# Optimization experiments

Hardware: AMD Instinct MI355X
Metric: run time of the kernel (lower is better)

## Reference

```python
import jax, jax.numpy as jnp
import numpy as np

N_FEATS = 512
SND = N_FEATS // 2
N_NODES = 100000
NUM_GRAPHS = 256
EPS = 1e-5


def graph_norm(x, batch, num_seg, w, b, ms):
    # PyG GraphNorm: out = w * (x - mean[batch]*mean_scale) / sqrt(var[batch]+eps) + b
    cnt = jax.ops.segment_sum(jnp.ones((x.shape[0],), x.dtype), batch, num_seg)
    cnt = jnp.maximum(cnt, 1.0)[:, None]
    mean = jax.ops.segment_sum(x, batch, num_seg) / cnt
    sub = x - mean[batch] * ms
    var = jax.ops.segment_sum(sub * sub, batch, num_seg) / cnt
    return w * sub * jax.lax.rsqrt(var[batch] + EPS) + b


def graph_norm_global(x, w, b, ms):
    # gn3 is called without `batch` in the source -> batch=None -> global stats
    mean = jnp.mean(x, axis=0, keepdims=True)
    sub = x - mean * ms
    var = jnp.mean(sub * sub, axis=0, keepdims=True)
    return w * sub * jax.lax.rsqrt(var + EPS) + b


def prelu(x, a):
    return jnp.where(x >= 0, x, a * x)


def linear(x, W, b):
    return x @ W.T + b


def setup_inputs() -> dict:
    key = jax.random.key(0)
    ks = jax.random.split(key, 12)
    d = {}
    d['x'] = jax.random.normal(ks[0], (N_NODES, N_FEATS), jnp.float32)
    d['batch'] = jnp.sort(jax.random.randint(ks[1], (N_NODES,), 0, NUM_GRAPHS)).astype(jnp.int64)
    # GraphNorm params (PyG init: weight=1, bias=0, mean_scale=1)
    for name, dim in [('gn1', N_FEATS), ('gn2', SND), ('gn3', SND), ('gn4', SND), ('gn5', SND)]:
        d[name + '_w'] = jnp.ones((dim,), jnp.float32)
        d[name + '_b'] = jnp.zeros((dim,), jnp.float32)
        d[name + '_ms'] = jnp.ones((dim,), jnp.float32)
    # Linear weights/biases
    d['lin1_W'] = jax.random.normal(ks[2], (SND, N_FEATS), jnp.float32) * 0.02
    d['lin1_b'] = jnp.zeros((SND,), jnp.float32)
    d['lin2_W'] = jax.random.normal(ks[3], (SND, SND), jnp.float32) * 0.02
    d['lin2_b'] = jnp.zeros((SND,), jnp.float32)
    d['lin3_W'] = jax.random.normal(ks[4], (SND, SND), jnp.float32) * 0.02
    d['lin3_b'] = jnp.zeros((SND,), jnp.float32)
    d['lin4_W'] = jax.random.normal(ks[5], (SND, SND), jnp.float32) * 0.02
    d['lin4_b'] = jnp.zeros((SND,), jnp.float32)
    d['lin5_W'] = jax.random.normal(ks[6], (N_FEATS, SND), jnp.float32) * 0.02
    d['lin5_b'] = jnp.zeros((N_FEATS,), jnp.float32)
    # PReLU params (single param, init 0.25)
    for name in ['a2', 'a3', 'a4', 'a5']:
        d[name] = jnp.full((1,), 0.25, jnp.float32)
    return d


def reference(x, batch,
              gn1_w, gn1_b, gn1_ms, gn2_w, gn2_b, gn2_ms, gn3_w, gn3_b, gn3_ms,
              gn4_w, gn4_b, gn4_ms, gn5_w, gn5_b, gn5_ms,
              lin1_W, lin1_b, lin2_W, lin2_b, lin3_W, lin3_b, lin4_W, lin4_b,
              lin5_W, lin5_b, a2, a3, a4, a5):
    # x = lin1(gn1(x, batch))
    x1 = linear(graph_norm(x, batch, NUM_GRAPHS, gn1_w, gn1_b, gn1_ms), lin1_W, lin1_b)
    # x = (lin3(gn3(lin2(gn2(x, batch)))) + x) / 2   [gn3 uses global stats]
    h = linear(prelu(graph_norm(x1, batch, NUM_GRAPHS, gn2_w, gn2_b, gn2_ms), a2), lin2_W, lin2_b)
    h = linear(prelu(graph_norm_global(h, gn3_w, gn3_b, gn3_ms), a3), lin3_W, lin3_b)
    x2 = (h + x1) / 2
    # x = (lin4(gn4(x, batch)) + x) / 2
    h = linear(prelu(graph_norm(x2, batch, NUM_GRAPHS, gn4_w, gn4_b, gn4_ms), a4), lin4_W, lin4_b)
    x3 = (h + x2) / 2
    # x = lin5(gn5(x, batch))
    out = linear(prelu(graph_norm(x3, batch, NUM_GRAPHS, gn5_w, gn5_b, gn5_ms), a5), lin5_W, lin5_b)
    return out
```

## Files before the change

### kernel.cpp

```cpp
#include <hip/hip_runtime.h>
#include <cstddef>
#include <cstdint>

#define NF 512
#define SND 256
#define NG 256
#define EPSV 1e-5f

typedef __attribute__((ext_vector_type(8))) short bf16x8;
typedef __attribute__((ext_vector_type(4))) float f32x4;

__device__ __forceinline__ float bf2f(unsigned short u) {
  return __uint_as_float(((unsigned int)u) << 16);
}
__device__ __forceinline__ unsigned short f2bf(float f) {
  unsigned int u = __float_as_uint(f);
  return (unsigned short)((u + 0x7fffu + ((u >> 16) & 1u)) >> 16);
}
__device__ __forceinline__ unsigned int pack2bf(float a, float b) {
  return (unsigned int)f2bf(a) | ((unsigned int)f2bf(b) << 16);
}

__device__ __forceinline__ void async16(const unsigned short* g, unsigned short* l) {
  __builtin_amdgcn_global_load_lds(
      (const __attribute__((address_space(1))) unsigned int*)g,
      (__attribute__((address_space(3))) unsigned int*)l, 16, 0, 0);
}

__global__ void offsets_kernel(const int* __restrict__ batch, int* __restrict__ offs, int M) {
  int t = threadIdx.x + blockIdx.x * blockDim.x;
  if (t > NG) return;
  if (t == NG) { offs[NG] = M; return; }
  int lo = 0, hi = M;
  while (lo < hi) { int mid = (lo + hi) >> 1; if (batch[mid] < t) lo = mid + 1; else hi = mid; }
  offs[t] = lo;
}

__global__ void wconv_kernel(const float* __restrict__ w1, const float* __restrict__ w2,
                             const float* __restrict__ w3, const float* __restrict__ w4,
                             const float* __restrict__ w5,
                             unsigned short* __restrict__ o1, unsigned short* __restrict__ o2,
                             unsigned short* __restrict__ o3, unsigned short* __restrict__ o4,
                             unsigned short* __restrict__ o5) {
  int i = threadIdx.x + blockIdx.x * 256;
  if (i < 131072) { o1[i] = f2bf(w1[i]); o5[i] = f2bf(w5[i]); }
  if (i < 65536)  { o2[i] = f2bf(w2[i]); o3[i] = f2bf(w3[i]); o4[i] = f2bf(w4[i]); }
}

template <typename T, int F, int VE, bool WB, bool GLOB>
__global__ void stats_k(const T* __restrict__ X, const int* __restrict__ offs, int M,
                        float* __restrict__ ps, float* __restrict__ pq,
                        unsigned short* __restrict__ xbf) {
  constexpr int TPR = F / VE, RPB = 256 / TPR;
  const int g = GLOB ? 0 : blockIdx.x;
  const int s = GLOB ? 0 : offs[g];
  const int e = GLOB ? M : offs[g + 1];
  const int slot = threadIdx.x / TPR;
  const int f0 = (threadIdx.x % TPR) * VE;
  float a0[VE], a1[VE];
#pragma unroll
  for (int i = 0; i < VE; ++i) { a0[i] = 0.f; a1[i] = 0.f; }

  for (int r = s + (int)blockIdx.y * RPB + slot; r < e; r += (int)gridDim.y * RPB) {
    float v[VE];
    if constexpr (sizeof(T) == 2) {
      const uint4 u = *(const uint4*)((const unsigned short*)X + (size_t)r * F + f0);
      v[0] = __uint_as_float(u.x << 16); v[1] = __uint_as_float(u.x & 0xffff0000u);
      v[2] = __uint_as_float(u.y << 16); v[3] = __uint_as_float(u.y & 0xffff0000u);
      v[4] = __uint_as_float(u.z << 16); v[5] = __uint_as_float(u.z & 0xffff0000u);
      v[6] = __uint_as_float(u.w << 16); v[7] = __uint_as_float(u.w & 0xffff0000u);
    } else {
      const float4 u = *(const float4*)((const float*)X + (size_t)r * F + f0);
      v[0] = u.x; v[1] = u.y; v[2] = u.z; v[3] = u.w;
    }
#pragma unroll
    for (int i = 0; i < VE; ++i) { a0[i] += v[i]; a1[i] += v[i] * v[i]; }
    if constexpr (WB) {
      *(uint2*)(xbf + (size_t)r * F + f0) = make_uint2(pack2bf(v[0], v[1]), pack2bf(v[2], v[3]));
    }
  }

  const int groups = GLOB ? 1 : (int)gridDim.x;
  const size_t pbase = (size_t)blockIdx.y * ((size_t)groups * F) + (size_t)g * F + f0;

  __shared__ float red[256 * VE];
  __syncthreads();
#pragma unroll
  for (int i = 0; i < VE; ++i) red[slot * F + f0 + i] = a0[i];
  __syncthreads();
  if (slot == 0) {
    float t[VE];
#pragma unroll
    for (int i = 0; i < VE; ++i) {
      t[i] = 0.f;
      for (int sl = 0; sl < RPB; ++sl) t[i] += red[sl * F + f0 + i];
    }
#pragma unroll
    for (int i = 0; i < VE; i += 4)
      *(float4*)&ps[pbase + i] = make_float4(t[i], t[i + 1], t[i + 2], t[i + 3]);
  }
  __syncthreads();
#pragma unroll
  for (int i = 0; i < VE; ++i) red[slot * F + f0 + i] = a1[i];
  __syncthreads();
  if (slot == 0) {
    float t[VE];
#pragma unroll
    for (int i = 0; i < VE; ++i) {
      t[i] = 0.f;
      for (int sl = 0; sl < RPB; ++sl) t[i] += red[sl * F + f0 + i];
    }
#pragma unroll
    for (int i = 0; i < VE; i += 4)
      *(float4*)&pq[pbase + i] = make_float4(t[i], t[i + 1], t[i + 2], t[i + 3]);
  }
}

__global__ void finalize_kernel(const float* __restrict__ ps, const float* __restrict__ pq,
                                const float* __restrict__ w, const float* __restrict__ b,
                                const float* __restrict__ ms, const int* __restrict__ offs,
                                int fixed_cnt, int F, int P,
                                float* __restrict__ sc, float* __restrict__ sh) {
  int idx = threadIdx.x + blockIdx.x * 256;
  int g = idx / F, f = idx - g * F;
  int total = (int)gridDim.x * 256;
  float s0 = 0.f, s1 = 0.f;
  for (int p = 0; p < P; ++p) {
    s0 += ps[(size_t)p * total + idx];
    s1 += pq[(size_t)p * total + idx];
  }
  float cnt = offs ? (float)(offs[g + 1] - offs[g]) : (float)fixed_cnt;
  cnt = fmaxf(cnt, 1.0f);
  float mean = s0 / cnt;
  float ex2  = s1 / cnt;
  float mm = mean * ms[f];
  float var = ex2 - 2.f * mm * mean + mm * mm;
  float rstd = rsqrtf(var + EPSV);
  float s = w[f] * rstd;
  sc[idx] = s;
  sh[idx] = b[f] - mm * s;
}

template <int K, bool PRELU, bool GLOB>
__global__ void norm_act(const unsigned short* __restrict__ Xin, unsigned short* __restrict__ Aout,
                         const float* __restrict__ SC, const float* __restrict__ SH,
                         const int* __restrict__ batch, const float* __restrict__ pa, int M) {
  constexpr int TPR = K / 8, RPB = 256 / TPR;
  const int row = blockIdx.x * RPB + threadIdx.x / TPR;
  if (row >= M) return;
  const int f0 = (threadIdx.x % TPR) * 8;
  const int g = GLOB ? 0 : batch[row];
  const float a = PRELU ? pa[0] : 0.f;
  const uint4 u = *(const uint4*)(Xin + (size_t)row * K + f0);
  const float4 s0 = *(const float4*)(SC + (size_t)g * K + f0);
  const float4 s1 = *(const float4*)(SC + (size_t)g * K + f0 + 4);
  const float4 h0 = *(const float4*)(SH + (size_t)g * K + f0);
  const float4 h1 = *(const float4*)(SH + (size_t)g * K + f0 + 4);
  float v[8];
  v[0] = __uint_as_float(u.x << 16); v[1] = __uint_as_float(u.x & 0xffff0000u);
  v[2] = __uint_as_float(u.y << 16); v[3] = __uint_as_float(u.y & 0xffff0000u);
  v[4] = __uint_as_float(u.z << 16); v[5] = __uint_as_float(u.z & 0xffff0000u);
  v[6] = __uint_as_float(u.w << 16); v[7] = __uint_as_float(u.w & 0xffff0000u);
  v[0] = fmaf(v[0], s0.x, h0.x); v[1] = fmaf(v[1], s0.y, h0.y);
  v[2] = fmaf(v[2], s0.z, h0.z); v[3] = fmaf(v[3], s0.w, h0.w);
  v[4] = fmaf(v[4], s1.x, h1.x); v[5] = fmaf(v[5], s1.y, h1.y);
  v[6] = fmaf(v[6], s1.z, h1.z); v[7] = fmaf(v[7], s1.w, h1.w);
  if (PRELU) {
#pragma unroll
    for (int i = 0; i < 8; ++i) v[i] = v[i] >= 0.f ? v[i] : a * v[i];
  }
  *(uint4*)(Aout + (size_t)row * K + f0) =
      make_uint4(pack2bf(v[0], v[1]), pack2bf(v[2], v[3]),
                 pack2bf(v[4], v[5]), pack2bf(v[6], v[7]));
}

template <int K, bool RESID, bool OUT_BF>
__global__ __launch_bounds__(256, 4)
void gemm_bf16(const unsigned short* __restrict__ A, const unsigned short* __restrict__ Bw,
               const float* __restrict__ lb_, const unsigned short* __restrict__ resid,
               void* __restrict__ outv, int M, int N) {
  __shared__ __align__(16) unsigned short sA[128 * 64];
  __shared__ __align__(16) unsigned short sB[128 * 64];
  const int tid = threadIdx.x;
  const int wave = tid >> 6, lane = tid & 63;
  const int m0 = blockIdx.y * 128, n0 = blockIdx.x * 128;
  const int wm = wave & 1, wn = wave >> 1;
  const int qd = lane >> 4, l15 = lane & 15;

  const int srow = lane >> 3;
  const int schunk = lane & 7;
  const int gchunk = schunk ^ srow;

  f32x4 acc[4][4];
#pragma unroll
  for (int mi = 0; mi < 4; ++mi)
#pragma unroll
    for (int ni = 0; ni < 4; ++ni) acc[mi][ni] = (f32x4){0.f, 0.f, 0.f, 0.f};

  const unsigned short* Abase = A + (size_t)m0 * K;
  const unsigned short* Bbase = Bw + (size_t)n0 * K;

  for (int kt = 0; kt < K / 64; ++kt) {
    const int kOff = kt * 64 + gchunk * 8;
#pragma unroll
    for (int i = 0; i < 4; ++i) {
      const int r = wave * 32 + i * 8 + srow;
      async16(Abase + (size_t)r * K + kOff, &sA[(wave * 4 + i) * 512]);
      async16(Bbase + (size_t)r * K + kOff, &sB[(wave * 4 + i) * 512]);
    }
    __syncthreads();
#pragma unroll
    for (int ks = 0; ks < 2; ++ks) {
      bf16x8 af[4], bfr[4];
      const int pc = ((ks * 4 + qd) ^ (l15 & 7)) * 8;
#pragma unroll
      for (int mi = 0; mi < 4; ++mi)
        af[mi] = *(const bf16x8*)&sA[(wm * 64 + mi * 16 + l15) * 64 + pc];
#pragma unroll
      for (int ni = 0; ni < 4; ++ni)
        bfr[ni] = *(const bf16x8*)&sB[(wn * 64 + ni * 16 + l15) * 64 + pc];
#pragma unroll
      for (int mi = 0; mi < 4; ++mi)
#pragma unroll
        for (int ni = 0; ni < 4; ++ni)
          acc[mi][ni] = __builtin_amdgcn_mfma_f32_16x16x32_bf16(af[mi], bfr[ni], acc[mi][ni], 0, 0, 0);
    }
    __syncthreads();
  }

  float lb[4];
#pragma unroll
  for (int ni = 0; ni < 4; ++ni) lb[ni] = lb_[n0 + wn * 64 + ni * 16 + l15];
  float* outF = (float*)outv;
  unsigned short* outH = (unsigned short*)outv;
#pragma unroll
  for (int mi = 0; mi < 4; ++mi) {
#pragma unroll
    for (int i = 0; i < 4; ++i) {
      const int row = m0 + wm * 64 + mi * 16 + qd * 4 + i;
      if (row >= M) continue;
#pragma unroll
      for (int ni = 0; ni < 4; ++ni) {
        const int col = n0 + wn * 64 + ni * 16 + l15;
        float v = acc[mi][ni][i] + lb[ni];
        if (RESID) v = 0.5f * (v + bf2f(resid[(size_t)row * N + col]));
        if (OUT_BF) outH[(size_t)row * N + col] = f2bf(v);
        else        outF[(size_t)row * N + col] = v;
      }
    }
  }
}

extern "C" void kernel_launch(void* const* d_in, const int* in_sizes, int n_in,
                              void* d_out, int out_size, void* d_ws, size_t ws_size,
                              hipStream_t stream) {
  const float* x    = (const float*)d_in[0];
  const int* batch  = (const int*)d_in[1];
  const float* gw1 = (const float*)d_in[2],  *gb1 = (const float*)d_in[3],  *gm1 = (const float*)d_in[4];
  const float* gw2 = (const float*)d_in[5],  *gb2 = (const float*)d_in[6],  *gm2 = (const float*)d_in[7];
  const float* gw3 = (const float*)d_in[8],  *gb3 = (const float*)d_in[9],  *gm3 = (const float*)d_in[10];
  const float* gw4 = (const float*)d_in[11], *gb4 = (const float*)d_in[12], *gm4 = (const float*)d_in[13];
  const float* gw5 = (const float*)d_in[14], *gb5 = (const float*)d_in[15], *gm5 = (const float*)d_in[16];
  const float* W1 = (const float*)d_in[17], *b1 = (const float*)d_in[18];
  const float* W2 = (const float*)d_in[19], *b2 = (const float*)d_in[20];
  const float* W3 = (const float*)d_in[21], *b3 = (const float*)d_in[22];
  const float* W4 = (const float*)d_in[23], *b4 = (const float*)d_in[24];
  const float* W5 = (const float*)d_in[25], *b5 = (const float*)d_in[26];
  const float* a2 = (const float*)d_in[27], *a3 = (const float*)d_in[28];
  const float* a4 = (const float*)d_in[29], *a5 = (const float*)d_in[30];
  float* out = (float*)d_out;
  (void)n_in; (void)out_size; (void)ws_size;

  const int M = in_sizes[0] / NF;
  const int MT = (M + 127) / 128;
  const int M_pad = MT * 128;

  char* wsp = (char*)d_ws;
  size_t off = 0;
  auto take = [&](size_t bytes) -> void* {
    void* p = wsp + off;
    off = (off + bytes + 255) & ~(size_t)255;
    return p;
  };
  int* offs            = (int*)take((NG + 1) * sizeof(int));
  unsigned short* Wb1  = (unsigned short*)take((size_t)SND * NF * 2);
  unsigned short* Wb2  = (unsigned short*)take((size_t)SND * SND * 2);
  unsigned short* Wb3  = (unsigned short*)take((size_t)SND * SND * 2);
  unsigned short* Wb4  = (unsigned short*)take((size_t)SND * SND * 2);
  unsigned short* Wb5  = (unsigned short*)take((size_t)NF * SND * 2);
  float* psum          = (float*)take((size_t)8 * NG * NF * 4);
  float* psq           = (float*)take((size_t)8 * NG * NF * 4);
  float* sc            = (float*)take((size_t)NG * NF * 4);
  float* sh            = (float*)take((size_t)NG * NF * 4);
  unsigned short* B1   = (unsigned short*)take((size_t)M_pad * SND * 2);
  unsigned short* B2   = (unsigned short*)take((size_t)M_pad * SND * 2);
  unsigned short* Abuf = (unsigned short*)take((size_t)M_pad * NF * 2);

  offsets_kernel<<<2, 256, 0, stream>>>(batch, offs, M);
  wconv_kernel<<<512, 256, 0, stream>>>(W1, W2, W3, W4, W5, Wb1, Wb2, Wb3, Wb4, Wb5);

  stats_k<float, NF, 4, true, false><<<dim3(NG, 8), 256, 0, stream>>>(x, offs, M, psum, psq, Abuf);
  finalize_kernel<<<(NG * NF) / 256, 256, 0, stream>>>(psum, psq, gw1, gb1, gm1, offs, M, NF, 8, sc, sh);
  norm_act<NF, false, false><<<(M + 3) / 4, 256, 0, stream>>>(Abuf, Abuf, sc, sh, batch, nullptr, M);
  gemm_bf16<NF, false, true><<<dim3(SND / 128, MT), 256, 0, stream>>>(Abuf, Wb1, b1, nullptr, B1, M, SND);

  stats_k<unsigned short, SND, 8, false, false><<<dim3(NG, 4), 256, 0, stream>>>(B1, offs, M, psum, psq, nullptr);
  finalize_kernel<<<(NG * SND) / 256, 256, 0, stream>>>(psum, psq, gw2, gb2, gm2, offs, M, SND, 4, sc, sh);
  norm_act<SND, true, false><<<(M + 7) / 8, 256, 0, stream>>>(B1, Abuf, sc, sh, batch, a2, M);
  gemm_bf16<SND, false, true><<<dim3(SND / 128, MT), 256, 0, stream>>>(Abuf, Wb2, b2, nullptr, B2, M, SND);

  stats_k<unsigned short, SND, 8, false, true><<<dim3(1, 512), 256, 0, stream>>>(B2, offs, M, psum, psq, nullptr);
  finalize_kernel<<<1, 256, 0, stream>>>(psum, psq, gw3, gb3, gm3, nullptr, M, SND, 512, sc, sh);
  norm_act<SND, true, true><<<(M + 7) / 8, 256, 0, stream>>>(B2, Abuf, sc, sh, nullptr, a3, M);
  gemm_bf16<SND, true, true><<<dim3(SND / 128, MT), 256, 0, stream>>>(Abuf, Wb3, b3, B1, B2, M, SND);

  stats_k<unsigned short, SND, 8, false, false><<<dim3(NG, 4), 256, 0, stream>>>(B2, offs, M, psum, psq, nullptr);
  finalize_kernel<<<(NG * SND) / 256, 256, 0, stream>>>(psum, psq, gw4, gb4, gm4, offs, M, SND, 4, sc, sh);
  norm_act<SND, true, false><<<(M + 7) / 8, 256, 0, stream>>>(B2, Abuf, sc, sh, batch, a4, M);
  gemm_bf16<SND, true, true><<<dim3(SND / 128, MT), 256, 0, stream>>>(Abuf, Wb4, b4, B2, B1, M, SND);

  stats_k<unsigned short, SND, 8, false, false><<<dim3(NG, 4), 256, 0, stream>>>(B1, offs, M, psum, psq, nullptr);
  finalize_kernel<<<(NG * SND) / 256, 256, 0, stream>>>(psum, psq, gw5, gb5, gm5, offs, M, SND, 4, sc, sh);
  norm_act<SND, true, false><<<(M + 7) / 8, 256, 0, stream>>>(B1, Abuf, sc, sh, batch, a5, M);
  gemm_bf16<SND, false, false><<<dim3(NF / 128, MT), 256, 0, stream>>>(Abuf, Wb5, b5, nullptr, out, M, NF);
}
```

Before: 912.1 us.

## Fuse finalize into stats via last-block atomics, merge prep kernels, remap GEMM tiles per XCD

After: 1.474 ms. 1.62x slower.

```diff
diff --git a/kernel.cpp b/kernel.cpp
--- a/kernel.cpp
+++ b/kernel.cpp
@@ -20,6 +20,12 @@
 __device__ __forceinline__ unsigned int pack2bf(float a, float b) {
   return (unsigned int)f2bf(a) | ((unsigned int)f2bf(b) << 16);
 }
+__device__ __forceinline__ void unpack8(const uint4 u, float* v) {
+  v[0] = __uint_as_float(u.x << 16); v[1] = __uint_as_float(u.x & 0xffff0000u);
+  v[2] = __uint_as_float(u.y << 16); v[3] = __uint_as_float(u.y & 0xffff0000u);
+  v[4] = __uint_as_float(u.z << 16); v[5] = __uint_as_float(u.z & 0xffff0000u);
+  v[6] = __uint_as_float(u.w << 16); v[7] = __uint_as_float(u.w & 0xffff0000u);
+}
 
 __device__ __forceinline__ void async16(const unsigned short* g, unsigned short* l) {
   __builtin_amdgcn_global_load_lds(
@@ -27,30 +33,36 @@
       (__attribute__((address_space(3))) unsigned int*)l, 16, 0, 0);
 }
 
-__global__ void offsets_kernel(const int* __restrict__ batch, int* __restrict__ offs, int M) {
-  int t = threadIdx.x + blockIdx.x * blockDim.x;
-  if (t > NG) return;
-  if (t == NG) { offs[NG] = M; return; }
-  int lo = 0, hi = M;
-  while (lo < hi) { int mid = (lo + hi) >> 1; if (batch[mid] < t) lo = mid + 1; else hi = mid; }
-  offs[t] = lo;
-}
-
-__global__ void wconv_kernel(const float* __restrict__ w1, const float* __restrict__ w2,
-                             const float* __restrict__ w3, const float* __restrict__ w4,
-                             const float* __restrict__ w5,
-                             unsigned short* __restrict__ o1, unsigned short* __restrict__ o2,
-                             unsigned short* __restrict__ o3, unsigned short* __restrict__ o4,
-                             unsigned short* __restrict__ o5) {
+__global__ void prep_kernel(const float* __restrict__ w1, const float* __restrict__ w2,
+                            const float* __restrict__ w3, const float* __restrict__ w4,
+                            const float* __restrict__ w5,
+                            unsigned short* __restrict__ o1, unsigned short* __restrict__ o2,
+                            unsigned short* __restrict__ o3, unsigned short* __restrict__ o4,
+                            unsigned short* __restrict__ o5,
+                            const int* __restrict__ batch, int* __restrict__ offs, int M,
+                            unsigned int* __restrict__ cnts) {
   int i = threadIdx.x + blockIdx.x * 256;
   if (i < 131072) { o1[i] = f2bf(w1[i]); o5[i] = f2bf(w5[i]); }
   if (i < 65536)  { o2[i] = f2bf(w2[i]); o3[i] = f2bf(w3[i]); o4[i] = f2bf(w4[i]); }
+  if (i < 5 * NG) cnts[i] = 0u;
+  if (i <= NG) {
+    if (i == NG) { offs[NG] = M; }
+    else {
+      int lo = 0, hi = M;
+      while (lo < hi) { int mid = (lo + hi) >> 1; if (batch[mid] < i) lo = mid + 1; else hi = mid; }
+      offs[i] = lo;
+    }
+  }
 }
 
 template <typename T, int F, int VE, bool WB, bool GLOB>
 __global__ void stats_k(const T* __restrict__ X, const int* __restrict__ offs, int M,
                         float* __restrict__ ps, float* __restrict__ pq,
-                        unsigned short* __restrict__ xbf) {
+                        unsigned short* __restrict__ xbf,
+                        const float* __restrict__ w, const float* __restrict__ bb,
+                        const float* __restrict__ ms,
+                        float* __restrict__ sc, float* __restrict__ sh,
+                        unsigned int* __restrict__ cnt) {
   constexpr int TPR = F / VE, RPB = 256 / TPR;
   const int g = GLOB ? 0 : blockIdx.x;
   const int s = GLOB ? 0 : offs[g];
@@ -65,10 +77,7 @@
     float v[VE];
     if constexpr (sizeof(T) == 2) {
       const uint4 u = *(const uint4*)((const unsigned short*)X + (size_t)r * F + f0);
-      v[0] = __uint_as_float(u.x << 16); v[1] = __uint_as_float(u.x & 0xffff0000u);
-      v[2] = __uint_as_float(u.y << 16); v[3] = __uint_as_float(u.y & 0xffff0000u);
-      v[4] = __uint_as_float(u.z << 16); v[5] = __uint_as_float(u.z & 0xffff0000u);
-      v[6] = __uint_as_float(u.w << 16); v[7] = __uint_as_float(u.w & 0xffff0000u);
+      unpack8(u, v);
     } else {
       const float4 u = *(const float4*)((const float*)X + (size_t)r * F + f0);
       v[0] = u.x; v[1] = u.y; v[2] = u.z; v[3] = u.w;
@@ -114,31 +123,35 @@
     for (int i = 0; i < VE; i += 4)
       *(float4*)&pq[pbase + i] = make_float4(t[i], t[i + 1], t[i + 2], t[i + 3]);
   }
-}
-
-__global__ void finalize_kernel(const float* __restrict__ ps, const float* __restrict__ pq,
-                                const float* __restrict__ w, const float* __restrict__ b,
-                                const float* __restrict__ ms, const int* __restrict__ offs,
-                                int fixed_cnt, int F, int P,
-                                float* __restrict__ sc, float* __restrict__ sh) {
-  int idx = threadIdx.x + blockIdx.x * 256;
-  int g = idx / F, f = idx - g * F;
-  int total = (int)gridDim.x * 256;
-  float s0 = 0.f, s1 = 0.f;
-  for (int p = 0; p < P; ++p) {
-    s0 += ps[(size_t)p * total + idx];
-    s1 += pq[(size_t)p * total + idx];
-  }
-  float cnt = offs ? (float)(offs[g + 1] - offs[g]) : (float)fixed_cnt;
-  cnt = fmaxf(cnt, 1.0f);
-  float mean = s0 / cnt;
-  float ex2  = s1 / cnt;
-  float mm = mean * ms[f];
-  float var = ex2 - 2.f * mm * mean + mm * mm;
-  float rstd = rsqrtf(var + EPSV);
-  float s = w[f] * rstd;
-  sc[idx] = s;
-  sh[idx] = b[f] - mm * s;
+
+  __shared__ bool lastBlk;
+  __threadfence();
+  __syncthreads();
+  if (threadIdx.x == 0)
+    lastBlk = (atomicAdd(&cnt[g], 1u) == (unsigned)gridDim.y - 1u);
+  __syncthreads();
+  if (!lastBlk) return;
+  __threadfence();
+
+  const int P = (int)gridDim.y;
+  const float cntf = fmaxf((float)(e - s), 1.0f);
+  const size_t stride = (size_t)groups * F;
+  for (int f = threadIdx.x; f < F; f += 256) {
+    float s0 = 0.f, s1 = 0.f;
+    const size_t base = (size_t)g * F + f;
+    for (int p = 0; p < P; ++p) {
+      s0 += ps[(size_t)p * stride + base];
+      s1 += pq[(size_t)p * stride + base];
+    }
+    float mean = s0 / cntf;
+    float ex2  = s1 / cntf;
+    float mm = mean * ms[f];
+    float var = ex2 - 2.f * mm * mean + mm * mm;
+    float rstd = rsqrtf(var + EPSV);
+    float sv = w[f] * rstd;
+    sc[g * F + f] = sv;
+    sh[g * F + f] = bb[f] - mm * sv;
+  }
 }
 
 template <int K, bool PRELU, bool GLOB>
@@ -157,10 +170,7 @@
   const float4 h0 = *(const float4*)(SH + (size_t)g * K + f0);
   const float4 h1 = *(const float4*)(SH + (size_t)g * K + f0 + 4);
   float v[8];
-  v[0] = __uint_as_float(u.x << 16); v[1] = __uint_as_float(u.x & 0xffff0000u);
-  v[2] = __uint_as_float(u.y << 16); v[3] = __uint_as_float(u.y & 0xffff0000u);
-  v[4] = __uint_as_float(u.z << 16); v[5] = __uint_as_float(u.z & 0xffff0000u);
-  v[6] = __uint_as_float(u.w << 16); v[7] = __uint_as_float(u.w & 0xffff0000u);
+  unpack8(u, v);
   v[0] = fmaf(v[0], s0.x, h0.x); v[1] = fmaf(v[1], s0.y, h0.y);
   v[2] = fmaf(v[2], s0.z, h0.z); v[3] = fmaf(v[3], s0.w, h0.w);
   v[4] = fmaf(v[4], s1.x, h1.x); v[5] = fmaf(v[5], s1.y, h1.y);
@@ -183,7 +193,17 @@
   __shared__ __align__(16) unsigned short sB[128 * 64];
   const int tid = threadIdx.x;
   const int wave = tid >> 6, lane = tid & 63;
-  const int m0 = blockIdx.y * 128, n0 = blockIdx.x * 128;
+
+  const int gx = (int)gridDim.x;
+  const int nwg = gx * (int)gridDim.y;
+  const int bid = (int)blockIdx.y * gx + (int)blockIdx.x;
+  const int q = nwg >> 3, r = nwg & 7;
+  const int xcd = bid & 7, ii = bid >> 3;
+  const int logical = (xcd < r) ? xcd * (q + 1) + ii : r * (q + 1) + (xcd - r) * q + ii;
+  const int bx = logical % gx;
+  const int by = logical / gx;
+
+  const int m0 = by * 128, n0 = bx * 128;
   const int wm = wave & 1, wn = wave >> 1;
   const int qd = lane >> 4, l15 = lane & 15;
 
@@ -204,9 +224,9 @@
     const int kOff = kt * 64 + gchunk * 8;
 #pragma unroll
     for (int i = 0; i < 4; ++i) {
-      const int r = wave * 32 + i * 8 + srow;
-      async16(Abase + (size_t)r * K + kOff, &sA[(wave * 4 + i) * 512]);
-      async16(Bbase + (size_t)r * K + kOff, &sB[(wave * 4 + i) * 512]);
+      const int r2 = wave * 32 + i * 8 + srow;
+      async16(Abase + (size_t)r2 * K + kOff, &sA[(wave * 4 + i) * 512]);
+      async16(Bbase + (size_t)r2 * K + kOff, &sB[(wave * 4 + i) * 512]);
     }
     __syncthreads();
 #pragma unroll
@@ -283,6 +303,7 @@
     return p;
   };
   int* offs            = (int*)take((NG + 1) * sizeof(int));
+  unsigned int* cnts   = (unsigned int*)take((size_t)5 * NG * sizeof(unsigned int));
   unsigned short* Wb1  = (unsigned short*)take((size_t)SND * NF * 2);
   unsigned short* Wb2  = (unsigned short*)take((size_t)SND * SND * 2);
   unsigned short* Wb3  = (unsigned short*)take((size_t)SND * SND * 2);
@@ -296,31 +317,31 @@
   unsigned short* B2   = (unsigned short*)take((size_t)M_pad * SND * 2);
   unsigned short* Abuf = (unsigned short*)take((size_t)M_pad * NF * 2);
 
-  offsets_kernel<<<2, 256, 0, stream>>>(batch, offs, M);
-  wconv_kernel<<<512, 256, 0, stream>>>(W1, W2, W3, W4, W5, Wb1, Wb2, Wb3, Wb4, Wb5);
-
-  stats_k<float, NF, 4, true, false><<<dim3(NG, 8), 256, 0, stream>>>(x, offs, M, psum, psq, Abuf);
-  finalize_kernel<<<(NG * NF) / 256, 256, 0, stream>>>(psum, psq, gw1, gb1, gm1, offs, M, NF, 8, sc, sh);
+  prep_kernel<<<512, 256, 0, stream>>>(W1, W2, W3, W4, W5, Wb1, Wb2, Wb3, Wb4, Wb5,
+                                       batch, offs, M, cnts);
+
+  stats_k<float, NF, 4, true, false><<<dim3(NG, 8), 256, 0, stream>>>(
+      x, offs, M, psum, psq, Abuf, gw1, gb1, gm1, sc, sh, cnts + 0 * NG);
   norm_act<NF, false, false><<<(M + 3) / 4, 256, 0, stream>>>(Abuf, Abuf, sc, sh, batch, nullptr, M);
   gemm_bf16<NF, false, true><<<dim3(SND / 128, MT), 256, 0, stream>>>(Abuf, Wb1, b1, nullptr, B1, M, SND);
 
-  stats_k<unsigned short, SND, 8, false, false><<<dim3(NG, 4), 256, 0, stream>>>(B1, offs, M, psum, psq, nullptr);
-  finalize_kernel<<<(NG * SND) / 256, 256, 0, stream>>>(psum, psq, gw2, gb2, gm2, offs, M, SND, 4, sc, sh);
+  stats_k<unsigned short, SND, 8, false, false><<<dim3(NG, 4), 256, 0, stream>>>(
+      B1, offs, M, psum, psq, nullptr, gw2, gb2, gm2, sc, sh, cnts + 1 * NG);
   norm_act<SND, true, false><<<(M + 7) / 8, 256, 0, stream>>>(B1, Abuf, sc, sh, batch, a2, M);
   gemm_bf16<SND, false, true><<<dim3(SND / 128, MT), 256, 0, stream>>>(Abuf, Wb2, b2, nullptr, B2, M, SND);
 
-  stats_k<unsigned short, SND, 8, false, true><<<dim3(1, 512), 256, 0, stream>>>(B2, offs, M, psum, psq, nullptr);
-  finalize_kernel<<<1, 256, 0, stream>>>(psum, psq, gw3, gb3, gm3, nullptr, M, SND, 512, sc, sh);
+  stats_k<unsigned short, SND, 8, false, true><<<dim3(1, 512), 256, 0, stream>>>(
+      B2, offs, M, psum, psq, nullptr, gw3, gb3, gm3, sc, sh, cnts + 2 * NG);
   norm_act<SND, true, true><<<(M + 7) / 8, 256, 0, stream>>>(B2, Abuf, sc, sh, nullptr, a3, M);
   gemm_bf16<SND, true, true><<<dim3(SND / 128, MT), 256, 0, stream>>>(Abuf, Wb3, b3, B1, B2, M, SND);
 
-  stats_k<unsigned short, SND, 8, false, false><<<dim3(NG, 4), 256, 0, stream>>>(B2, offs, M, psum, psq, nullptr);
-  finalize_kernel<<<(NG * SND) / 256, 256, 0, stream>>>(psum, psq, gw4, gb4, gm4, offs, M, SND, 4, sc, sh);
+  stats_k<unsigned short, SND, 8, false, false><<<dim3(NG, 4), 256, 0, stream>>>(
+      B2, offs, M, psum, psq, nullptr, gw4, gb4, gm4, sc, sh, cnts + 3 * NG);
   norm_act<SND, true, false><<<(M + 7) / 8, 256, 0, stream>>>(B2, Abuf, sc, sh, batch, a4, M);
   gemm_bf16<SND, true, true><<<dim3(SND / 128, MT), 256, 0, stream>>>(Abuf, Wb4, b4, B2, B1, M, SND);
 
-  stats_k<unsigned short, SND, 8, false, false><<<dim3(NG, 4), 256, 0, stream>>>(B1, offs, M, psum, psq, nullptr);
-  finalize_kernel<<<(NG * SND) / 256, 256, 0, stream>>>(psum, psq, gw5, gb5, gm5, offs, M, SND, 4, sc, sh);
+  stats_k<unsigned short, SND, 8, false, false><<<dim3(NG, 4), 256, 0, stream>>>(
+      B1, offs, M, psum, psq, nullptr, gw5, gb5, gm5, sc, sh, cnts + 4 * NG);
   norm_act<SND, true, false><<<(M + 7) / 8, 256, 0, stream>>>(B1, Abuf, sc, sh, batch, a5, M);
   gemm_bf16<SND, false, false><<<dim3(NF / 128, MT), 256, 0, stream>>>(Abuf, Wb5, b5, nullptr, out, M, NF);
 }
```
